# Kernel tuning notes

Hardware: AMD Instinct MI355X
Metric: run time of the kernel (lower is better)

Reference implementation:

```python
import jax, jax.numpy as jnp
import numpy as np

N, F, O, E = 2048, 128, 128, 16


def setup_inputs() -> dict:
    key = jax.random.key(0)
    ks = jax.random.split(key, 6)
    x = jax.random.normal(ks[0], (N, F), dtype=jnp.float32)
    # two supports (normalized adjacency-like dense matrices)
    support = jax.random.uniform(ks[1], (2, N, N), dtype=jnp.float32)
    edge_feature = jax.random.normal(ks[2], (N, N, E), dtype=jnp.float32)
    # glorot-ish scale for edge weight and dense weights
    weight_edge = jax.random.normal(ks[3], (N, N, E), dtype=jnp.float32) * 0.05
    bias_edge = jnp.zeros((N, N), dtype=jnp.float32)
    glorot = float(np.sqrt(6.0 / (F + O)))
    w0 = jax.random.uniform(ks[4], (F, O), dtype=jnp.float32, minval=-glorot, maxval=glorot)
    w1 = jax.random.uniform(ks[5], (F, O), dtype=jnp.float32, minval=-glorot, maxval=glorot)
    b = jnp.zeros((O,), dtype=jnp.float32)
    return {"x": x, "support": support, "edge_feature": edge_feature,
            "weight_edge": weight_edge, "bias_edge": bias_edge,
            "w0": w0, "w1": w1, "b": b}


def reference(x, support, edge_feature, weight_edge, bias_edge, w0, w1, b):
    # support branch 0: plain GCN propagation  (SpMM expressed dense)
    pre0 = x @ w0                      # [N, O]
    s0 = support[0] @ pre0             # [N, O]
    # support branch 1: edge-feature gated propagation
    pre1 = x @ w1                      # [N, O]
    # per-pair dot of edge features with per-pair weights -> [N, N] gate
    edge = jax.nn.sigmoid(jnp.einsum('nme,nme->nm', edge_feature, weight_edge) + bias_edge)
    s1 = (edge * support[1]) @ pre1    # gated adjacency matmul, [N, O]
    out = s0 + s1 + b                  # add_n + bias
    return jax.nn.relu(out)
```

## Files before the change

kernel.cpp:

```cpp
#include <hip/hip_runtime.h>
#include <math.h>

#define N 2048
#define F 128
#define O 128
#define E 16

typedef __attribute__((ext_vector_type(8))) short          shortx8;
typedef __attribute__((ext_vector_type(8))) unsigned short u16x8;
typedef __attribute__((ext_vector_type(4))) unsigned short u16x4;
typedef __attribute__((ext_vector_type(4))) float          floatx4;

static __device__ __forceinline__ unsigned short f2bf(float f) {
    unsigned int u = __float_as_uint(f);
    unsigned int r = (u + 0x7FFFu + ((u >> 16) & 1u)) >> 16;
    return (unsigned short)r;
}

__global__ __launch_bounds__(256)
void pre_t(const float* __restrict__ x,
           const float* __restrict__ w0,
           const float* __restrict__ w1,
           unsigned short* __restrict__ preT) {
    __shared__ unsigned short wT[128 * 136];
    const int t  = threadIdx.x;
    const int n0 = blockIdx.x * 16;
    const int b  = blockIdx.y;
    const float* __restrict__ wsrc = b ? w1 : w0;

#pragma unroll
    for (int i = 0; i < 64; ++i) {
        const int idx = i * 256 + t;
        const int k = idx >> 7, o = idx & 127;
        wT[o * 136 + k] = f2bf(wsrc[idx]);
    }
    __syncthreads();

    const int lane = t & 63;
    const int wv   = t >> 6;
    const int row  = lane & 15;
    const int kg   = lane >> 4;
    const int col0 = wv * 32 + row;

    floatx4 acc0 = {0.f, 0.f, 0.f, 0.f};
    floatx4 acc1 = {0.f, 0.f, 0.f, 0.f};

#pragma unroll
    for (int kk = 0; kk < 4; ++kk) {
        const float* xp = x + (size_t)(n0 + row) * F + kk * 32 + kg * 8;
        const float4 f0 = *(const float4*)(xp);
        const float4 f1 = *(const float4*)(xp + 4);
        shortx8 a;
        a[0] = (short)f2bf(f0.x); a[1] = (short)f2bf(f0.y);
        a[2] = (short)f2bf(f0.z); a[3] = (short)f2bf(f0.w);
        a[4] = (short)f2bf(f1.x); a[5] = (short)f2bf(f1.y);
        a[6] = (short)f2bf(f1.z); a[7] = (short)f2bf(f1.w);
        const shortx8 bA = *(const shortx8*)(wT + col0 * 136 + kk * 32 + kg * 8);
        const shortx8 bB = *(const shortx8*)(wT + (col0 + 16) * 136 + kk * 32 + kg * 8);
        acc0 = __builtin_amdgcn_mfma_f32_16x16x32_bf16(a, bA, acc0, 0, 0, 0);
        acc1 = __builtin_amdgcn_mfma_f32_16x16x32_bf16(a, bB, acc1, 0, 0, 0);
    }

    const int prow = kg * 4;
    u16x4 s0, s1;
#pragma unroll
    for (int j = 0; j < 4; ++j) { s0[j] = f2bf(acc0[j]); s1[j] = f2bf(acc1[j]); }
    *(u16x4*)(preT + ((size_t)b * O + col0) * N + n0 + prow)      = s0;
    *(u16x4*)(preT + ((size_t)b * O + col0 + 16) * N + n0 + prow) = s1;
}

__global__ __launch_bounds__(256)
void gate_kernel(const float* __restrict__ ef,
                 const float* __restrict__ we,
                 const float* __restrict__ be,
                 const float* __restrict__ sup1,
                 const float* __restrict__ S0,
                 unsigned short* __restrict__ G,
                 unsigned short* __restrict__ S0bf) {
    const size_t tid  = (size_t)blockIdx.x * 256 + threadIdx.x;
    const size_t pair = tid >> 2;
    const int    sub  = (int)(threadIdx.x & 3);
    const float4 e4 = ((const float4*)ef)[pair * 4 + sub];
    const float4 w4 = ((const float4*)we)[pair * 4 + sub];
    float v = e4.x * w4.x + e4.y * w4.y + e4.z * w4.z + e4.w * w4.w;
    v += __shfl_xor(v, 1);
    v += __shfl_xor(v, 2);
    if (sub == 0) {
        const float t = v + be[pair];
        const float g = (1.f / (1.f + __expf(-t))) * sup1[pair];
        G[pair] = f2bf(g);
    } else if (sub == 1) {
        S0bf[pair] = f2bf(S0[pair]);
    }
}

__global__ __launch_bounds__(1024, 4)
void gemm_direct(const unsigned short* __restrict__ S0bf,
                 const unsigned short* __restrict__ G,
                 const unsigned short* __restrict__ preT,
                 const float* __restrict__ bias,
                 float* __restrict__ out) {
    __shared__ float red[16][16][36];

    const int bx   = blockIdx.x;
    const int orig = (bx & 7) * 64 + (bx >> 3);
    const int rb   = orig >> 2;
    const int cg   = orig & 3;
    const int n0   = rb * 16;

    const int t    = threadIdx.x;
    const int lane = t & 63;
    const int wv   = t >> 6;
    const int m_b  = wv * 128;
    const int row  = lane & 15;
    const int kg   = lane >> 4;
    const int col0 = cg * 32 + row;

    const unsigned short* aS = S0bf + (size_t)(n0 + row) * N + m_b + kg * 8;
    const unsigned short* aG = G    + (size_t)(n0 + row) * N + m_b + kg * 8;
    const unsigned short* b0 = preT + (size_t)col0 * N        + m_b + kg * 8;
    const unsigned short* b1 = b0 + (size_t)16 * N;
    const unsigned short* c0 = b0 + (size_t)O * N;
    const unsigned short* c1 = b1 + (size_t)O * N;

    shortx8 As[4], Ag[4], B00[4], B01[4], B10[4], B11[4];
#pragma unroll
    for (int s = 0; s < 4; ++s) {
        const int mo = s * 32;
        As[s]  = *(const shortx8*)(aS + mo);
        Ag[s]  = *(const shortx8*)(aG + mo);
        B00[s] = *(const shortx8*)(b0 + mo);
        B01[s] = *(const shortx8*)(b1 + mo);
        B10[s] = *(const shortx8*)(c0 + mo);
        B11[s] = *(const shortx8*)(c1 + mo);
    }

    floatx4 acc0 = {0.f, 0.f, 0.f, 0.f};
    floatx4 acc1 = {0.f, 0.f, 0.f, 0.f};
#pragma unroll
    for (int s = 0; s < 4; ++s) {
        acc0 = __builtin_amdgcn_mfma_f32_16x16x32_bf16(As[s], B00[s], acc0, 0, 0, 0);
        acc0 = __builtin_amdgcn_mfma_f32_16x16x32_bf16(Ag[s], B10[s], acc0, 0, 0, 0);
        acc1 = __builtin_amdgcn_mfma_f32_16x16x32_bf16(As[s], B01[s], acc1, 0, 0, 0);
        acc1 = __builtin_amdgcn_mfma_f32_16x16x32_bf16(Ag[s], B11[s], acc1, 0, 0, 0);
    }

    const int prow = kg * 4;
#pragma unroll
    for (int j = 0; j < 4; ++j) {
        red[wv][prow + j][row]      = acc0[j];
        red[wv][prow + j][16 + row] = acc1[j];
    }
    __syncthreads();

    if (t < 256) {
        const int r = t >> 4;
        const int c = (t & 15) * 2;
        float v0 = 0.f, v1 = 0.f;
#pragma unroll
        for (int w = 0; w < 16; ++w) {
            v0 += red[w][r][c];
            v1 += red[w][r][c + 1];
        }
        v0 = fmaxf(v0 + bias[cg * 32 + c],     0.f);
        v1 = fmaxf(v1 + bias[cg * 32 + c + 1], 0.f);
        float2 o2; o2.x = v0; o2.y = v1;
        *(float2*)(out + (size_t)(n0 + r) * O + cg * 32 + c) = o2;
    }
}

extern "C" void kernel_launch(void* const* d_in, const int* in_sizes, int n_in,
                              void* d_out, int out_size, void* d_ws, size_t ws_size,
                              hipStream_t stream) {
    const float* x   = (const float*)d_in[0];
    const float* sup = (const float*)d_in[1];
    const float* ef  = (const float*)d_in[2];
    const float* we  = (const float*)d_in[3];
    const float* be  = (const float*)d_in[4];
    const float* w0  = (const float*)d_in[5];
    const float* w1  = (const float*)d_in[6];
    const float* b   = (const float*)d_in[7];
    float* out = (float*)d_out;

    unsigned short* preT = (unsigned short*)d_ws;
    unsigned short* G    = preT + 2 * (size_t)N * O;
    unsigned short* S0bf = G + (size_t)N * N;

    pre_t<<<dim3(N / 16, 2), 256, 0, stream>>>(x, w0, w1, preT);
    gate_kernel<<<(unsigned)((size_t)N * N * 4 / 256), 256, 0, stream>>>(
        ef, we, be, sup + (size_t)N * N, sup, G, S0bf);
    gemm_direct<<<512, 1024, 0, stream>>>(S0bf, G, preT, b, out);
}
```

Baseline: 133.0 us.

## Read fp32 support0 directly in GEMM and split-K into partial buffers

```diff
diff --git a/kernel.cpp b/kernel.cpp
--- a/kernel.cpp
+++ b/kernel.cpp
@@ -74,9 +74,7 @@
                  const float* __restrict__ we,
                  const float* __restrict__ be,
                  const float* __restrict__ sup1,
-                 const float* __restrict__ S0,
-                 unsigned short* __restrict__ G,
-                 unsigned short* __restrict__ S0bf) {
+                 unsigned short* __restrict__ G) {
     const size_t tid  = (size_t)blockIdx.x * 256 + threadIdx.x;
     const size_t pair = tid >> 2;
     const int    sub  = (int)(threadIdx.x & 3);
@@ -89,45 +87,45 @@
         const float t = v + be[pair];
         const float g = (1.f / (1.f + __expf(-t))) * sup1[pair];
         G[pair] = f2bf(g);
-    } else if (sub == 1) {
-        S0bf[pair] = f2bf(S0[pair]);
-    }
-}
-
-__global__ __launch_bounds__(1024, 4)
-void gemm_direct(const unsigned short* __restrict__ S0bf,
-                 const unsigned short* __restrict__ G,
-                 const unsigned short* __restrict__ preT,
-                 const float* __restrict__ bias,
-                 float* __restrict__ out) {
-    __shared__ float red[16][16][36];
+    }
+}
+
+__global__ __launch_bounds__(256, 3)
+void gemm_partial(const float* __restrict__ S0,
+                  const unsigned short* __restrict__ G,
+                  const unsigned short* __restrict__ preT,
+                  float* __restrict__ partial) {
+    __shared__ float red[4][16][36];
 
     const int bx   = blockIdx.x;
-    const int orig = (bx & 7) * 64 + (bx >> 3);
-    const int rb   = orig >> 2;
-    const int cg   = orig & 3;
+    const int orig = (bx & 7) * 256 + (bx >> 3);
+    const int rb   = orig >> 4;
+    const int cg   = (orig >> 2) & 3;
+    const int kc   = orig & 3;
     const int n0   = rb * 16;
 
     const int t    = threadIdx.x;
     const int lane = t & 63;
     const int wv   = t >> 6;
-    const int m_b  = wv * 128;
+    const int m_b  = kc * 512 + wv * 128;
     const int row  = lane & 15;
     const int kg   = lane >> 4;
     const int col0 = cg * 32 + row;
 
-    const unsigned short* aS = S0bf + (size_t)(n0 + row) * N + m_b + kg * 8;
+    const float*          aS = S0   + (size_t)(n0 + row) * N + m_b + kg * 8;
     const unsigned short* aG = G    + (size_t)(n0 + row) * N + m_b + kg * 8;
     const unsigned short* b0 = preT + (size_t)col0 * N        + m_b + kg * 8;
     const unsigned short* b1 = b0 + (size_t)16 * N;
     const unsigned short* c0 = b0 + (size_t)O * N;
     const unsigned short* c1 = b1 + (size_t)O * N;
 
-    shortx8 As[4], Ag[4], B00[4], B01[4], B10[4], B11[4];
+    float4  Af0[4], Af1[4];
+    shortx8 Ag[4], B00[4], B01[4], B10[4], B11[4];
 #pragma unroll
     for (int s = 0; s < 4; ++s) {
         const int mo = s * 32;
-        As[s]  = *(const shortx8*)(aS + mo);
+        Af0[s] = *(const float4*)(aS + mo);
+        Af1[s] = *(const float4*)(aS + mo + 4);
         Ag[s]  = *(const shortx8*)(aG + mo);
         B00[s] = *(const shortx8*)(b0 + mo);
         B01[s] = *(const shortx8*)(b1 + mo);
@@ -139,9 +137,14 @@
     floatx4 acc1 = {0.f, 0.f, 0.f, 0.f};
 #pragma unroll
     for (int s = 0; s < 4; ++s) {
-        acc0 = __builtin_amdgcn_mfma_f32_16x16x32_bf16(As[s], B00[s], acc0, 0, 0, 0);
+        shortx8 a_s;
+        a_s[0] = (short)f2bf(Af0[s].x); a_s[1] = (short)f2bf(Af0[s].y);
+        a_s[2] = (short)f2bf(Af0[s].z); a_s[3] = (short)f2bf(Af0[s].w);
+        a_s[4] = (short)f2bf(Af1[s].x); a_s[5] = (short)f2bf(Af1[s].y);
+        a_s[6] = (short)f2bf(Af1[s].z); a_s[7] = (short)f2bf(Af1[s].w);
+        acc0 = __builtin_amdgcn_mfma_f32_16x16x32_bf16(a_s,   B00[s], acc0, 0, 0, 0);
         acc0 = __builtin_amdgcn_mfma_f32_16x16x32_bf16(Ag[s], B10[s], acc0, 0, 0, 0);
-        acc1 = __builtin_amdgcn_mfma_f32_16x16x32_bf16(As[s], B01[s], acc1, 0, 0, 0);
+        acc1 = __builtin_amdgcn_mfma_f32_16x16x32_bf16(a_s,   B01[s], acc1, 0, 0, 0);
         acc1 = __builtin_amdgcn_mfma_f32_16x16x32_bf16(Ag[s], B11[s], acc1, 0, 0, 0);
     }
 
@@ -153,20 +156,34 @@
     }
     __syncthreads();
 
-    if (t < 256) {
+    {
         const int r = t >> 4;
         const int c = (t & 15) * 2;
-        float v0 = 0.f, v1 = 0.f;
-#pragma unroll
-        for (int w = 0; w < 16; ++w) {
-            v0 += red[w][r][c];
-            v1 += red[w][r][c + 1];
-        }
-        v0 = fmaxf(v0 + bias[cg * 32 + c],     0.f);
-        v1 = fmaxf(v1 + bias[cg * 32 + c + 1], 0.f);
+        float v0 = red[0][r][c]     + red[1][r][c]     + red[2][r][c]     + red[3][r][c];
+        float v1 = red[0][r][c + 1] + red[1][r][c + 1] + red[2][r][c + 1] + red[3][r][c + 1];
         float2 o2; o2.x = v0; o2.y = v1;
-        *(float2*)(out + (size_t)(n0 + r) * O + cg * 32 + c) = o2;
-    }
+        *(float2*)(partial + (size_t)kc * (N * O)
+                   + (size_t)(n0 + r) * O + cg * 32 + c) = o2;
+    }
+}
+
+__global__ __launch_bounds__(256)
+void reduce_out(const float* __restrict__ partial,
+                const float* __restrict__ bias,
+                float* __restrict__ out) {
+    const int i4 = blockIdx.x * 256 + threadIdx.x;
+    const float4* p = (const float4*)partial;
+    const float4 a = p[i4];
+    const float4 b = p[i4 + 65536];
+    const float4 c = p[i4 + 2 * 65536];
+    const float4 d = p[i4 + 3 * 65536];
+    const float4 bb = ((const float4*)bias)[i4 & 31];
+    float4 r;
+    r.x = fmaxf(a.x + b.x + c.x + d.x + bb.x, 0.f);
+    r.y = fmaxf(a.y + b.y + c.y + d.y + bb.y, 0.f);
+    r.z = fmaxf(a.z + b.z + c.z + d.z + bb.z, 0.f);
+    r.w = fmaxf(a.w + b.w + c.w + d.w + bb.w, 0.f);
+    ((float4*)out)[i4] = r;
 }
 
 extern "C" void kernel_launch(void* const* d_in, const int* in_sizes, int n_in,
@@ -182,12 +199,13 @@
     const float* b   = (const float*)d_in[7];
     float* out = (float*)d_out;
 
-    unsigned short* preT = (unsigned short*)d_ws;
-    unsigned short* G    = preT + 2 * (size_t)N * O;
-    unsigned short* S0bf = G + (size_t)N * N;
+    unsigned short* preT   = (unsigned short*)d_ws;
+    unsigned short* G      = preT + 2 * (size_t)N * O;
+    float*          partial = (float*)(G + (size_t)N * N);
 
     pre_t<<<dim3(N / 16, 2), 256, 0, stream>>>(x, w0, w1, preT);
     gate_kernel<<<(unsigned)((size_t)N * N * 4 / 256), 256, 0, stream>>>(
-        ef, we, be, sup + (size_t)N * N, sup, G, S0bf);
-    gemm_direct<<<512, 1024, 0, stream>>>(S0bf, G, preT, b, out);
-}
+        ef, we, be, sup + (size_t)N * N, G);
+    gemm_partial<<<2048, 256, 0, stream>>>(sup, G, preT, partial);
+    reduce_out<<<N * O / 4 / 256, 256, 0, stream>>>(partial, b, out);
+}
```

Result: slower. 141.6 us (+6.5%).
